# Kernel tuning notes

Measured on AMD Instinct MI355X. Metric: run time of the kernel, lower is better.

The kernel has to match this reference:

```python
import jax, jax.numpy as jnp
import numpy as np

N = 100000
E = 1600000
IN_DIM, HID, HEADS, OUT_DIM = 128, 64, 4, 40
NEG_SLOPE = 0.2
BN_EPS = 1e-5


def gat_conv(x, src, dst, W, att_src, att_dst, bias, heads, out_c, concat):
    # x: [N, F_in]; src/dst: [E'] (self-loops included)
    h = (x @ W).reshape(-1, heads, out_c)                      # [N, H, C]
    a_src = jnp.sum(h * att_src[None], axis=-1)                # [N, H]
    a_dst = jnp.sum(h * att_dst[None], axis=-1)                # [N, H]
    e = jax.nn.leaky_relu(a_src[src] + a_dst[dst], NEG_SLOPE)  # [E', H]
    # segment softmax over destination neighborhoods
    m = jax.ops.segment_max(e, dst, num_segments=N)            # [N, H]
    e = jnp.exp(e - m[dst])
    s = jax.ops.segment_sum(e, dst, num_segments=N)            # [N, H]
    alpha = e / (s[dst] + 1e-16)                               # [E', H]
    msg = h[src] * alpha[:, :, None]                           # [E', H, C]
    out = jax.ops.segment_sum(msg, dst, num_segments=N)        # [N, H, C]
    out = out.reshape(N, heads * out_c) if concat else out.mean(axis=1)
    return out + bias


def batch_norm(x, g, b, m, v):
    return (x - m) * (g / jnp.sqrt(v + BN_EPS)) + b


def setup_inputs() -> dict:
    key = jax.random.key(0)
    ks = jax.random.split(key, 16)
    rn = lambda k, shp, s=0.1: jax.random.normal(k, shp, jnp.float32) * s
    inp = {}
    inp['x'] = jax.random.normal(ks[0], (N, IN_DIM), jnp.float32)
    inp['edge_index'] = jax.random.randint(ks[1], (2, E), 0, N, jnp.int64)
    inp['W1'] = rn(ks[2], (IN_DIM, HEADS * HID))
    inp['att_src1'] = rn(ks[3], (HEADS, HID))
    inp['att_dst1'] = rn(ks[4], (HEADS, HID))
    inp['b1'] = rn(ks[5], (HEADS * HID,))
    inp['bn1_g'] = jax.random.uniform(ks[6], (HEADS * HID,), jnp.float32)
    inp['bn1_b'] = rn(ks[7], (HEADS * HID,))
    inp['bn1_m'] = jnp.zeros((HEADS * HID,), jnp.float32)
    inp['bn1_v'] = jnp.ones((HEADS * HID,), jnp.float32)
    inp['W2'] = rn(ks[8], (HEADS * HID, HID))
    inp['att_src2'] = rn(ks[9], (1, HID))
    inp['att_dst2'] = rn(ks[10], (1, HID))
    inp['b2'] = rn(ks[11], (HID,))
    inp['bn2_g'] = jax.random.uniform(ks[12], (HID,), jnp.float32)
    inp['bn2_b'] = rn(ks[13], (HID,))
    inp['bn2_m'] = jnp.zeros((HID,), jnp.float32)
    inp['bn2_v'] = jnp.ones((HID,), jnp.float32)
    inp['W3'] = rn(ks[14], (HID, OUT_DIM))
    k3 = jax.random.split(ks[15], 3)
    inp['att_src3'] = rn(k3[0], (1, OUT_DIM))
    inp['att_dst3'] = rn(k3[1], (1, OUT_DIM))
    inp['b3'] = rn(k3[2], (OUT_DIM,))
    return inp


def reference(x, edge_index, W1, att_src1, att_dst1, b1, bn1_g, bn1_b, bn1_m, bn1_v,
              W2, att_src2, att_dst2, b2, bn2_g, bn2_b, bn2_m, bn2_v,
              W3, att_src3, att_dst3, b3):
    # add self-loops (PyG GATConv default)
    loop = jnp.arange(N, dtype=edge_index.dtype)
    src = jnp.concatenate([edge_index[0], loop])
    dst = jnp.concatenate([edge_index[1], loop])
    # eval mode: dropout = identity, BN uses running stats
    h = gat_conv(x, src, dst, W1, att_src1, att_dst1, b1, HEADS, HID, True)
    h = jax.nn.elu(batch_norm(h, bn1_g, bn1_b, bn1_m, bn1_v))
    h = gat_conv(h, src, dst, W2, att_src2, att_dst2, b2, 1, HID, False)
    h = jax.nn.elu(batch_norm(h, bn2_g, bn2_b, bn2_m, bn2_v))
    out = gat_conv(h, src, dst, W3, att_src3, att_dst3, b3, 1, OUT_DIM, False)
    return jax.nn.log_softmax(out, axis=1)
```

## Files before the change

kernel.cpp:

```cpp
#include <hip/hip_runtime.h>
#include <hip/hip_fp16.h>
#include <cstdint>

#define IN_DIM   128
#define HIDC     64
#define HEADS    4
#define OUT_DIM  40
#define NEG_SLOPE 0.2f
#define BN_EPS   1e-5f

typedef unsigned short ushortt;
typedef float fx4 __attribute__((ext_vector_type(4)));

__device__ __forceinline__ float bfval(ushortt u) {
    return __uint_as_float(((unsigned)u) << 16);
}
__device__ __forceinline__ ushortt f2bf(float f) {
    unsigned u = __float_as_uint(f);
    u += 0x7fffu + ((u >> 16) & 1u);
    return (ushortt)(u >> 16);
}
__device__ __forceinline__ unsigned pack2bf(float a, float b) {
    return (unsigned)f2bf(a) | ((unsigned)f2bf(b) << 16);
}

__device__ __forceinline__ void acc8(float* acc, float a, uint4 h) {
    unsigned u;
    u = h.x;
    acc[0] = fmaf(a, __uint_as_float(u << 16), acc[0]);
    acc[1] = fmaf(a, __uint_as_float(u & 0xffff0000u), acc[1]);
    u = h.y;
    acc[2] = fmaf(a, __uint_as_float(u << 16), acc[2]);
    acc[3] = fmaf(a, __uint_as_float(u & 0xffff0000u), acc[3]);
    u = h.z;
    acc[4] = fmaf(a, __uint_as_float(u << 16), acc[4]);
    acc[5] = fmaf(a, __uint_as_float(u & 0xffff0000u), acc[5]);
    u = h.w;
    acc[6] = fmaf(a, __uint_as_float(u << 16), acc[6]);
    acc[7] = fmaf(a, __uint_as_float(u & 0xffff0000u), acc[7]);
}

__global__ void detect_kernel(const unsigned int* __restrict__ e, int* __restrict__ flag) {
    __shared__ int any;
    if (threadIdx.x == 0) any = 0;
    __syncthreads();
    for (int i = threadIdx.x; i < 1024; i += 256)
        if (e[2 * i + 1] != 0u) any = 1;
    __syncthreads();
    if (threadIdx.x == 0) flag[0] = any ? 0 : 1;
}

__device__ __forceinline__ int load_idx(const int* ei, int is64, long long pos) {
    return is64 ? ei[2 * pos] : ei[pos];
}

__global__ void hist_kernel(const int* __restrict__ ei, const int* __restrict__ flag,
                            int* __restrict__ deg, int E, int Etot) {
    int i = blockIdx.x * 256 + threadIdx.x;
    if (i >= Etot) return;
    int is64 = flag[0];
    int dst = (i < E) ? load_idx(ei, is64, (long long)E + i) : (i - E);
    atomicAdd(&deg[dst], 1);
}

__global__ void scan_kernel(int* __restrict__ data, int n) {
    __shared__ int wsum[16];
    __shared__ int chunk_total;
    int lane = threadIdx.x & 63;
    int w = threadIdx.x >> 6;
    int carry = 0;
    for (int base = 0; base < n; base += 1024) {
        int i = base + (int)threadIdx.x;
        int v = (i < n) ? data[i] : 0;
        int x = v;
        #pragma unroll
        for (int ofs = 1; ofs < 64; ofs <<= 1) {
            int y = __shfl_up(x, ofs);
            if (lane >= ofs) x += y;
        }
        if (lane == 63) wsum[w] = x;
        __syncthreads();
        if (w == 0) {
            int s = (lane < 16) ? wsum[lane] : 0;
            #pragma unroll
            for (int ofs = 1; ofs < 16; ofs <<= 1) {
                int y = __shfl_up(s, ofs);
                if (lane >= ofs) s += y;
            }
            if (lane < 16) wsum[lane] = s;
            if (lane == 15) chunk_total = s;
        }
        __syncthreads();
        int woff = (w > 0) ? wsum[w - 1] : 0;
        if (i < n) data[i] = (x + woff) - v + carry;
        int ct = chunk_total;
        __syncthreads();
        carry += ct;
    }
}

__global__ void scatter_kernel(const int* __restrict__ ei, const int* __restrict__ flag,
                               int* __restrict__ cursor, int* __restrict__ csr,
                               int* __restrict__ dstv, int E, int Etot) {
    int i = blockIdx.x * 256 + threadIdx.x;
    if (i >= Etot) return;
    int is64 = flag[0];
    int src, dst;
    if (i < E) {
        src = load_idx(ei, is64, i);
        dst = load_idx(ei, is64, (long long)E + i);
    } else {
        src = dst = i - E;
    }
    int pos = atomicAdd(&cursor[dst], 1);
    csr[pos] = src;
    dstv[pos] = dst;
}

__global__ void prep_bn_kernel(const float* b1, const float* g1, const float* bb1,
                               const float* m1, const float* v1,
                               const float* b2, const float* g2, const float* bb2,
                               const float* m2, const float* v2,
                               float* __restrict__ bnsc, float* __restrict__ bnsh) {
    int t = threadIdx.x;
    if (t < 256) {
        float s = g1[t] * rsqrtf(v1[t] + BN_EPS);
        bnsc[t] = s;
        bnsh[t] = (b1[t] - m1[t]) * s + bb1[t];
    } else if (t < 320) {
        int c = t - 256;
        float s = g2[c] * rsqrtf(v2[c] + BN_EPS);
        bnsc[t] = s;
        bnsh[t] = (b2[c] - m2[c]) * s + bb2[c];
    }
}

template <int K, int BN, int TN, int NC, int LDW, bool ABF16, bool L1MODE>
__launch_bounds__(256)
__global__ void gemm_fused_kernel(const void* __restrict__ Av, const float* __restrict__ W,
                                  ushortt* __restrict__ hB,
                                  const float* __restrict__ atts, const float* __restrict__ attd,
                                  float* __restrict__ a_s, float* __restrict__ a_d, int M) {
    __shared__ float Al[8][128];
    __shared__ float Wl[8][BN];
    int m0 = blockIdx.x * 128;
    int n0 = blockIdx.y * BN;
    int t = threadIdx.x;
    int tm = t >> 4, tn = t & 15;
    float acc[8][TN] = {};
    int r = t >> 1, kq = (t & 1) * 4;

    for (int k0 = 0; k0 < K; k0 += 8) {
        if constexpr (ABF16) {
            const ushortt* A = (const ushortt*)Av;
            uint2 av = make_uint2(0u, 0u);
            if (m0 + r < M) av = *(const uint2*)(A + (size_t)(m0 + r) * K + k0 + kq);
            Al[kq + 0][r] = bfval((ushortt)(av.x & 0xffffu));
            Al[kq + 1][r] = bfval((ushortt)(av.x >> 16));
            Al[kq + 2][r] = bfval((ushortt)(av.y & 0xffffu));
            Al[kq + 3][r] = bfval((ushortt)(av.y >> 16));
        } else {
            const float* A = (const float*)Av;
            float4 av = make_float4(0.f, 0.f, 0.f, 0.f);
            if (m0 + r < M) av = *(const float4*)&A[(size_t)(m0 + r) * K + k0 + kq];
            Al[kq + 0][r] = av.x; Al[kq + 1][r] = av.y;
            Al[kq + 2][r] = av.z; Al[kq + 3][r] = av.w;
        }
        if constexpr (BN == 128) {
            int kk = t >> 5, c4 = (t & 31) * 4;
            *(float4*)&Wl[kk][c4] = *(const float4*)&W[(size_t)(k0 + kk) * LDW + n0 + c4];
        } else {
            int kk = t >> 5, c2 = (t & 31) * 2;
            float2 wv = make_float2(0.f, 0.f);
            if (c2 + 2 <= NC) wv = *(const float2*)&W[(size_t)(k0 + kk) * LDW + n0 + c2];
            *(float2*)&Wl[kk][c2] = wv;
        }
        __syncthreads();
        #pragma unroll
        for (int k = 0; k < 8; ++k) {
            float4 a0 = *(const float4*)&Al[k][tm * 8];
            float4 a1 = *(const float4*)&Al[k][tm * 8 + 4];
            float aa[8] = {a0.x, a0.y, a0.z, a0.w, a1.x, a1.y, a1.z, a1.w};
            if constexpr (TN == 8) {
                float4 w0 = *(const float4*)&Wl[k][tn * 4];
                float4 w1 = *(const float4*)&Wl[k][64 + tn * 4];
                float ww[8] = {w0.x, w0.y, w0.z, w0.w, w1.x, w1.y, w1.z, w1.w};
                #pragma unroll
                for (int i = 0; i < 8; ++i)
                    #pragma unroll
                    for (int j = 0; j < 8; ++j)
                        acc[i][j] = fmaf(aa[i], ww[j], acc[i][j]);
            } else {
                float4 w0 = *(const float4*)&Wl[k][tn * 4];
                float ww[4] = {w0.x, w0.y, w0.z, w0.w};
                #pragma unroll
                for (int i = 0; i < 8; ++i)
                    #pragma unroll
                    for (int j = 0; j < 4; ++j)
                        acc[i][j] = fmaf(aa[i], ww[j], acc[i][j]);
            }
        }
        __syncthreads();
    }
    #pragma unroll
    for (int i = 0; i < 8; ++i) {
        int m = m0 + tm * 8 + i;
        bool valid = m < M;
        if constexpr (L1MODE) {
            int h0 = n0 >> 6;
            if (valid) {
                ushortt* row = hB + (size_t)m * 256 + n0;
                *(uint2*)(row + tn * 4) = make_uint2(pack2bf(acc[i][0], acc[i][1]),
                                                     pack2bf(acc[i][2], acc[i][3]));
                *(uint2*)(row + 64 + tn * 4) = make_uint2(pack2bf(acc[i][4], acc[i][5]),
                                                          pack2bf(acc[i][6], acc[i][7]));
            }
            int c0 = n0 + tn * 4, c1 = c0 + 64;
            float ps0 = acc[i][0] * atts[c0] + acc[i][1] * atts[c0 + 1]
                      + acc[i][2] * atts[c0 + 2] + acc[i][3] * atts[c0 + 3];
            float pd0 = acc[i][0] * attd[c0] + acc[i][1] * attd[c0 + 1]
                      + acc[i][2] * attd[c0 + 2] + acc[i][3] * attd[c0 + 3];
            float ps1 = acc[i][4] * atts[c1] + acc[i][5] * atts[c1 + 1]
                      + acc[i][6] * atts[c1 + 2] + acc[i][7] * atts[c1 + 3];
            float pd1 = acc[i][4] * attd[c1] + acc[i][5] * attd[c1 + 1]
                      + acc[i][6] * attd[c1 + 2] + acc[i][7] * attd[c1 + 3];
            #pragma unroll
            for (int o = 1; o < 16; o <<= 1) {
                ps0 += __shfl_xor(ps0, o); pd0 += __shfl_xor(pd0, o);
                ps1 += __shfl_xor(ps1, o); pd1 += __shfl_xor(pd1, o);
            }
            if (tn == 0 && valid) {
                a_s[(size_t)m * 4 + h0]     = ps0;
                a_s[(size_t)m * 4 + h0 + 1] = ps1;
                a_d[(size_t)m * 4 + h0]     = pd0;
                a_d[(size_t)m * 4 + h0 + 1] = pd1;
            }
        } else {
            if (valid) {
                ushortt* row = hB + (size_t)m * 64 + tn * 4;
                *(uint2*)row = make_uint2(pack2bf(acc[i][0], acc[i][1]),
                                          pack2bf(acc[i][2], acc[i][3]));
            }
            float ps = 0.f, pd = 0.f;
            #pragma unroll
            for (int j = 0; j < 4; ++j) {
                int c = tn * 4 + j;
                float as = (c < NC) ? atts[c] : 0.f;
                float ad = (c < NC) ? attd[c] : 0.f;
                ps = fmaf(acc[i][j], as, ps);
                pd = fmaf(acc[i][j], ad, pd);
            }
            #pragma unroll
            for (int o = 1; o < 16; o <<= 1) {
                ps += __shfl_xor(ps, o); pd += __shfl_xor(pd, o);
            }
            if (tn == 0 && valid) { a_s[m] = ps; a_d[m] = pd; }
        }
    }
}

__launch_bounds__(256)
__global__ void alpha4e_kernel(const int* __restrict__ csr, const int* __restrict__ dstv,
                               const float* __restrict__ a_s4, const float* __restrict__ a_d4,
                               __half* __restrict__ alH, int Etot) {
    int j = blockIdx.x * 256 + threadIdx.x;
    if (j >= Etot) return;
    int s = csr[j], d = dstv[j];
    fx4 as = *(const fx4*)&a_s4[(size_t)s * 4];
    fx4 ad = *(const fx4*)&a_d4[(size_t)d * 4];
    #pragma unroll
    for (int h = 0; h < 4; ++h) {
        float v = as[h] + ad[h];
        v = v > 0.f ? v : NEG_SLOPE * v;
        alH[(size_t)h * Etot + j] = __float2half(__expf(v));
    }
}

__launch_bounds__(256)
__global__ void pv1_kernel(const int* __restrict__ off, const int* __restrict__ csr,
                           const __half* __restrict__ alH, const ushortt* __restrict__ hB,
                           const float* __restrict__ bnsc, const float* __restrict__ bnsh,
                           ushortt* __restrict__ actb, int N, int Etot) {
    int node = blockIdx.x * 4 + (threadIdx.x >> 6);
    int lane = threadIdx.x & 63;
    if (node >= N) return;
    int half = lane >> 5, sub = lane & 31, head = sub >> 3;
    unsigned subb = (unsigned)(sub * 16);
    int beg = off[node], end = off[node + 1], deg = end - beg;
    const __half* alh = alH + (size_t)head * Etot;
    const char* hBb = (const char*)hB;
    float acc[8] = {};
    float ssum = 0.f;
    int nt = (deg + 1) >> 1;
    int j = beg + half;
    int t = 0;
    for (; t + 4 <= nt; t += 4, j += 8) {
        float av[4]; unsigned ro[4];
        #pragma unroll
        for (int q = 0; q < 4; ++q) {
            int jq = j + 2 * q;
            bool v = jq < end;
            int idx = v ? jq : beg;
            int s = csr[idx];
            av[q] = v ? __half2float(alh[idx]) : 0.f;
            ro[q] = (unsigned)s * 512u + subb;
        }
        uint4 h0 = *(const uint4*)(hBb + ro[0]);
        uint4 h1 = *(const uint4*)(hBb + ro[1]);
        uint4 h2 = *(const uint4*)(hBb + ro[2]);
        uint4 h3 = *(const uint4*)(hBb + ro[3]);
        acc8(acc, av[0], h0);
        acc8(acc, av[1], h1);
        acc8(acc, av[2], h2);
        acc8(acc, av[3], h3);
        ssum += (av[0] + av[1]) + (av[2] + av[3]);
    }
    for (; t < nt; ++t, j += 2) {
        bool v = j < end;
        int idx = v ? j : beg;
        int s = csr[idx];
        float a = v ? __half2float(alh[idx]) : 0.f;
        uint4 h = *(const uint4*)(hBb + (unsigned)s * 512u + subb);
        acc8(acc, a, h);
        ssum += a;
    }
    #pragma unroll
    for (int i = 0; i < 8; ++i) acc[i] += __shfl_xor(acc[i], 32);
    ssum += __shfl_xor(ssum, 32);
    if (half == 0) {
        float inv = 1.f / (ssum + 1e-16f);
        int g = sub * 8;
        float o[8];
        #pragma unroll
        for (int i = 0; i < 8; ++i) {
            float v = acc[i] * inv * bnsc[g + i] + bnsh[g + i];
            o[i] = v > 0.f ? v : expm1f(v);
        }
        uint4 pk = make_uint4(pack2bf(o[0], o[1]), pack2bf(o[2], o[3]),
                              pack2bf(o[4], o[5]), pack2bf(o[6], o[7]));
        *(uint4*)&actb[(size_t)node * 256 + g] = pk;
    }
}

__launch_bounds__(256)
__global__ void pv2_kernel(const int* __restrict__ off, const int* __restrict__ csr,
                           const float* __restrict__ a_s, const float* __restrict__ a_d,
                           const ushortt* __restrict__ hB,
                           const float* __restrict__ bnsc, const float* __restrict__ bnsh,
                           ushortt* __restrict__ act2b, int N) {
    int node = blockIdx.x * 4 + (threadIdx.x >> 6);
    int lane = threadIdx.x & 63;
    if (node >= N) return;
    int grp = lane >> 3, sub = lane & 7;
    unsigned subb = (unsigned)(sub * 16);
    int beg = off[node], end = off[node + 1], deg = end - beg;
    float ad = a_d[node];
    const char* hBb = (const char*)hB;
    float acc[8] = {};
    float ssum = 0.f;
    int nt = (deg + 7) >> 3;
    int j = beg + grp;
    int t = 0;
    for (; t + 2 <= nt; t += 2, j += 16) {
        int jA = j, jB = j + 8;
        bool vA = jA < end, vB = jB < end;
        int iA = vA ? jA : beg, iB = vB ? jB : beg;
        int sA = csr[iA], sB = csr[iB];
        float wA = a_s[sA] + ad; wA = wA > 0.f ? wA : NEG_SLOPE * wA;
        float wB = a_s[sB] + ad; wB = wB > 0.f ? wB : NEG_SLOPE * wB;
        float aA = vA ? __expf(wA) : 0.f;
        float aB = vB ? __expf(wB) : 0.f;
        uint4 hA = *(const uint4*)(hBb + (unsigned)sA * 128u + subb);
        uint4 hBv = *(const uint4*)(hBb + (unsigned)sB * 128u + subb);
        acc8(acc, aA, hA);
        acc8(acc, aB, hBv);
        ssum += aA + aB;
    }
    for (; t < nt; ++t, j += 8) {
        bool v = j < end;
        int idx = v ? j : beg;
        int s = csr[idx];
        float w = a_s[s] + ad; w = w > 0.f ? w : NEG_SLOPE * w;
        float a = v ? __expf(w) : 0.f;
        uint4 h = *(const uint4*)(hBb + (unsigned)s * 128u + subb);
        acc8(acc, a, h);
        ssum += a;
    }
    #pragma unroll
    for (int o = 8; o <= 32; o <<= 1) {
        #pragma unroll
        for (int i = 0; i < 8; ++i) acc[i] += __shfl_xor(acc[i], o);
        ssum += __shfl_xor(ssum, o);
    }
    if (lane < 8) {
        float inv = 1.f / (ssum + 1e-16f);
        int g = lane * 8;
        float o[8];
        #pragma unroll
        for (int i = 0; i < 8; ++i) {
            float v = acc[i] * inv * bnsc[256 + g + i] + bnsh[256 + g + i];
            o[i] = v > 0.f ? v : expm1f(v);
        }
        uint4 pk = make_uint4(pack2bf(o[0], o[1]), pack2bf(o[2], o[3]),
                              pack2bf(o[4], o[5]), pack2bf(o[6], o[7]));
        *(uint4*)&act2b[(size_t)node * 64 + g] = pk;
    }
}

__launch_bounds__(256)
__global__ void pv3_kernel(const int* __restrict__ off, const int* __restrict__ csr,
                           const float* __restrict__ a_s, const float* __restrict__ a_d,
                           const ushortt* __restrict__ hB, const float* __restrict__ bias,
                           float* __restrict__ out, int N) {
    int node = blockIdx.x * 4 + (threadIdx.x >> 6);
    int lane = threadIdx.x & 63;
    if (node >= N) return;
    int grp = lane >> 3, sub = lane & 7;
    unsigned subb = (unsigned)(sub * 16);
    int beg = off[node], end = off[node + 1];
    float ad = a_d[node];
    const char* hBb = (const char*)hB;
    float acc[8] = {};
    float ssum = 0.f;
    for (int j0 = beg; j0 < end; j0 += 8) {
        int j = j0 + grp;
        bool v = j < end;
        int idx = v ? j : beg;
        int s = csr[idx];
        float w = a_s[s] + ad; w = w > 0.f ? w : NEG_SLOPE * w;
        float a = v ? __expf(w) : 0.f;
        uint4 h = *(const uint4*)(hBb + (unsigned)s * 128u + subb);
        acc8(acc, a, h);
        ssum += a;
    }
    #pragma unroll
    for (int o = 8; o <= 32; o <<= 1) {
        #pragma unroll
        for (int i = 0; i < 8; ++i) acc[i] += __shfl_xor(acc[i], o);
        ssum += __shfl_xor(ssum, o);
    }
    float inv = 1.f / (ssum + 1e-16f);
    int g = lane * 8;
    bool act8 = lane < 5;
    float val[8];
    float mx = -INFINITY;
    #pragma unroll
    for (int i = 0; i < 8; ++i) {
        val[i] = act8 ? (acc[i] * inv + bias[act8 ? (g + i) : 0]) : -INFINITY;
        mx = fmaxf(mx, val[i]);
    }
    #pragma unroll
    for (int o = 1; o < 8; o <<= 1) mx = fmaxf(mx, __shfl_xor(mx, o));
    float se = 0.f;
    if (act8) {
        #pragma unroll
        for (int i = 0; i < 8; ++i) se += __expf(val[i] - mx);
    }
    #pragma unroll
    for (int o = 1; o < 8; o <<= 1) se += __shfl_xor(se, o);
    if (act8) {
        float lse = mx + logf(se);
        float* dst = &out[(size_t)node * 40 + g];
        fx4 v0 = {val[0] - lse, val[1] - lse, val[2] - lse, val[3] - lse};
        fx4 v1 = {val[4] - lse, val[5] - lse, val[6] - lse, val[7] - lse};
        *(fx4*)dst = v0;
        *(fx4*)(dst + 4) = v1;
    }
}

extern "C" void kernel_launch(void* const* d_in, const int* in_sizes, int n_in,
                              void* d_out, int out_size, void* d_ws, size_t ws_size,
                              hipStream_t stream) {
    const float* x      = (const float*)d_in[0];
    const int*   ei     = (const int*)d_in[1];
    const float* W1     = (const float*)d_in[2];
    const float* att_s1 = (const float*)d_in[3];
    const float* att_d1 = (const float*)d_in[4];
    const float* b1     = (const float*)d_in[5];
    const float* bn1g   = (const float*)d_in[6];
    const float* bn1b   = (const float*)d_in[7];
    const float* bn1m   = (const float*)d_in[8];
    const float* bn1v   = (const float*)d_in[9];
    const float* W2     = (const float*)d_in[10];
    const float* att_s2 = (const float*)d_in[11];
    const float* att_d2 = (const float*)d_in[12];
    const float* b2     = (const float*)d_in[13];
    const float* bn2g   = (const float*)d_in[14];
    const float* bn2b   = (const float*)d_in[15];
    const float* bn2m   = (const float*)d_in[16];
    const float* bn2v   = (const float*)d_in[17];
    const float* W3     = (const float*)d_in[18];
    const float* att_s3 = (const float*)d_in[19];
    const float* att_d3 = (const float*)d_in[20];
    const float* b3     = (const float*)d_in[21];

    const int N    = in_sizes[0] / IN_DIM;
    const int E    = in_sizes[1] / 2;
    const int Etot = E + N;

    int*   wsi = (int*)d_ws;
    float* wsf = (float*)d_ws;
    size_t p = 0;
    int*   off    = wsi + p; p += (size_t)N + 16;  p = (p + 3) & ~(size_t)3;
    int*   cursor = wsi + p; p += (size_t)N;       p = (p + 3) & ~(size_t)3;
    int*   flag   = wsi + p; p += 16;
    int*   csr    = wsi + p; p += (size_t)Etot;    p = (p + 3) & ~(size_t)3;
    int*   dstv   = wsi + p; p += (size_t)Etot;    p = (p + 3) & ~(size_t)3;
    float* a_s4   = wsf + p; p += (size_t)N * 4;
    float* a_d4   = wsf + p; p += (size_t)N * 4;
    float* bnsc   = wsf + p; p += 384;
    float* bnsh   = wsf + p; p += 384;
    size_t H = p;            p += (size_t)N * 128;
    size_t A1 = p;           p += (size_t)N * 128;
    size_t A2 = p;           p += (size_t)N * 32;
    __half* alH = (__half*)(wsf + p); p += (size_t)Etot * 2 + 16;
    if (ws_size < p * 4) return;

    ushortt* hB1   = (ushortt*)(wsf + H);
    ushortt* hB23  = (ushortt*)(wsf + H);
    ushortt* actb  = (ushortt*)(wsf + A1);
    ushortt* act2b = (ushortt*)(wsf + A2);

    float* outp = (float*)d_out;

    hipMemsetAsync(off, 0, ((size_t)N + 1) * sizeof(int), stream);
    detect_kernel<<<1, 256, 0, stream>>>((const unsigned int*)ei, flag);
    {
        int blocks = (Etot + 255) / 256;
        hist_kernel<<<blocks, 256, 0, stream>>>(ei, flag, off, E, Etot);
        scan_kernel<<<1, 1024, 0, stream>>>(off, N + 1);
        hipMemcpyAsync(cursor, off, (size_t)N * sizeof(int), hipMemcpyDeviceToDevice, stream);
        scatter_kernel<<<blocks, 256, 0, stream>>>(ei, flag, cursor, csr, dstv, E, Etot);
    }
    prep_bn_kernel<<<1, 384, 0, stream>>>(b1, bn1g, bn1b, bn1m, bn1v,
                                          b2, bn2g, bn2b, bn2m, bn2v, bnsc, bnsh);

    const int gm = (N + 127) / 128;
    const int nb4 = (N + 3) / 4;
    const int eb = (Etot + 255) / 256;

    gemm_fused_kernel<128, 128, 8, 256, 256, false, true>
        <<<dim3(gm, 2), 256, 0, stream>>>(x, W1, hB1, att_s1, att_d1, a_s4, a_d4, N);
    alpha4e_kernel<<<eb, 256, 0, stream>>>(csr, dstv, a_s4, a_d4, alH, Etot);
    pv1_kernel<<<nb4, 256, 0, stream>>>(off, csr, alH, hB1, bnsc, bnsh, actb, N, Etot);

    gemm_fused_kernel<256, 64, 4, 64, 64, true, false>
        <<<dim3(gm, 1), 256, 0, stream>>>(actb, W2, hB23, att_s2, att_d2, a_s4, a_d4, N);
    pv2_kernel<<<nb4, 256, 0, stream>>>(off, csr, a_s4, a_d4, hB23, bnsc, bnsh, act2b, N);

    gemm_fused_kernel<64, 64, 4, 40, 40, true, false>
        <<<dim3(gm, 1), 256, 0, stream>>>(act2b, W3, hB23, att_s3, att_d3, a_s4, a_d4, N);
    pv3_kernel<<<nb4, 256, 0, stream>>>(off, csr, a_s4, a_d4, hB23, b3, outp, N);
}
```

Measured before the change: 776.0 us.

## Use bf16 MFMA for GAT linear layers and precompute per-edge attention weights

Replaces the FP32 register-tiled GEMMs with a bf16 MFMA 16x16x32 kernel. To feed it, x is cast to bf16 and the weights are transposed and cast. Layers 2 and 3 now compute exp(leaky_relu) per edge in a separate pass stored as fp16, instead of recomputing it inside the aggregation kernels. This cuts FP32 FMA cost in the GEMMs and removes the gather of a_s plus the exp in the aggregation loops. In exchange it adds extra launches, extra edge-array traffic, and bf16 rounding of the input x.

Result: faster. 704.4 us (-9.2%).

```diff
diff --git a/kernel.cpp b/kernel.cpp
--- a/kernel.cpp
+++ b/kernel.cpp
@@ -11,6 +11,7 @@
 
 typedef unsigned short ushortt;
 typedef float fx4 __attribute__((ext_vector_type(4)));
+typedef short bf16x8 __attribute__((ext_vector_type(8)));
 
 __device__ __forceinline__ float bfval(ushortt u) {
     return __uint_as_float(((unsigned)u) << 16);
@@ -135,126 +136,96 @@
     }
 }
 
-template <int K, int BN, int TN, int NC, int LDW, bool ABF16, bool L1MODE>
+__global__ void castx_kernel(const float* __restrict__ x, ushortt* __restrict__ xb, int n8) {
+    int i = blockIdx.x * 256 + threadIdx.x;
+    if (i >= n8) return;
+    const float4* src = (const float4*)(x + (size_t)i * 8);
+    float4 v0 = src[0], v1 = src[1];
+    uint4 pk = make_uint4(pack2bf(v0.x, v0.y), pack2bf(v0.z, v0.w),
+                          pack2bf(v1.x, v1.y), pack2bf(v1.z, v1.w));
+    *(uint4*)(xb + (size_t)i * 8) = pk;
+}
+
+__global__ void prep_wt_kernel(const float* __restrict__ W, ushortt* __restrict__ WT,
+                               int K, int Norig, int Npad) {
+    int i = blockIdx.x * 256 + threadIdx.x;
+    if (i >= K * Npad) return;
+    int n = i / K, k = i % K;
+    WT[i] = (n < Norig) ? f2bf(W[(size_t)k * Norig + n]) : (ushortt)0;
+}
+
+template <int K, int NCATT, bool L1MODE>
 __launch_bounds__(256)
-__global__ void gemm_fused_kernel(const void* __restrict__ Av, const float* __restrict__ W,
-                                  ushortt* __restrict__ hB,
-                                  const float* __restrict__ atts, const float* __restrict__ attd,
-                                  float* __restrict__ a_s, float* __restrict__ a_d, int M) {
-    __shared__ float Al[8][128];
-    __shared__ float Wl[8][BN];
-    int m0 = blockIdx.x * 128;
-    int n0 = blockIdx.y * BN;
+__global__ void gemm_mfma_kernel(const ushortt* __restrict__ A, const ushortt* __restrict__ BT,
+                                 ushortt* __restrict__ hB,
+                                 const float* __restrict__ atts, const float* __restrict__ attd,
+                                 float* __restrict__ a_s, float* __restrict__ a_d, int M) {
+    __shared__ ushortt Abuf[64][40];
+    __shared__ ushortt Bbuf[64][40];
+    int m0 = blockIdx.x * 64;
+    int head = L1MODE ? blockIdx.y : 0;
+    int n0g = head * 64;
     int t = threadIdx.x;
-    int tm = t >> 4, tn = t & 15;
-    float acc[8][TN] = {};
-    int r = t >> 1, kq = (t & 1) * 4;
-
-    for (int k0 = 0; k0 < K; k0 += 8) {
-        if constexpr (ABF16) {
-            const ushortt* A = (const ushortt*)Av;
-            uint2 av = make_uint2(0u, 0u);
-            if (m0 + r < M) av = *(const uint2*)(A + (size_t)(m0 + r) * K + k0 + kq);
-            Al[kq + 0][r] = bfval((ushortt)(av.x & 0xffffu));
-            Al[kq + 1][r] = bfval((ushortt)(av.x >> 16));
-            Al[kq + 2][r] = bfval((ushortt)(av.y & 0xffffu));
-            Al[kq + 3][r] = bfval((ushortt)(av.y >> 16));
-        } else {
-            const float* A = (const float*)Av;
-            float4 av = make_float4(0.f, 0.f, 0.f, 0.f);
-            if (m0 + r < M) av = *(const float4*)&A[(size_t)(m0 + r) * K + k0 + kq];
-            Al[kq + 0][r] = av.x; Al[kq + 1][r] = av.y;
-            Al[kq + 2][r] = av.z; Al[kq + 3][r] = av.w;
-        }
-        if constexpr (BN == 128) {
-            int kk = t >> 5, c4 = (t & 31) * 4;
-            *(float4*)&Wl[kk][c4] = *(const float4*)&W[(size_t)(k0 + kk) * LDW + n0 + c4];
-        } else {
-            int kk = t >> 5, c2 = (t & 31) * 2;
-            float2 wv = make_float2(0.f, 0.f);
-            if (c2 + 2 <= NC) wv = *(const float2*)&W[(size_t)(k0 + kk) * LDW + n0 + c2];
-            *(float2*)&Wl[kk][c2] = wv;
-        }
+    int w = t >> 6, l = t & 63;
+    int colg = l & 15, kg = l >> 4;
+    int srow = t >> 2, sseg = t & 3;
+
+    fx4 acc[4] = {};
+
+    for (int k0 = 0; k0 < K; k0 += 32) {
+        uint4 av = make_uint4(0u, 0u, 0u, 0u);
+        if (m0 + srow < M)
+            av = *(const uint4*)(A + (size_t)(m0 + srow) * K + k0 + sseg * 8);
+        *(uint4*)&Abuf[srow][sseg * 8] = av;
+        uint4 bv = *(const uint4*)(BT + (size_t)(n0g + srow) * K + k0 + sseg * 8);
+        *(uint4*)&Bbuf[srow][sseg * 8] = bv;
         __syncthreads();
-        #pragma unroll
-        for (int k = 0; k < 8; ++k) {
-            float4 a0 = *(const float4*)&Al[k][tm * 8];
-            float4 a1 = *(const float4*)&Al[k][tm * 8 + 4];
-            float aa[8] = {a0.x, a0.y, a0.z, a0.w, a1.x, a1.y, a1.z, a1.w};
-            if constexpr (TN == 8) {
-                float4 w0 = *(const float4*)&Wl[k][tn * 4];
-                float4 w1 = *(const float4*)&Wl[k][64 + tn * 4];
-                float ww[8] = {w0.x, w0.y, w0.z, w0.w, w1.x, w1.y, w1.z, w1.w};
-                #pragma unroll
-                for (int i = 0; i < 8; ++i)
-                    #pragma unroll
-                    for (int j = 0; j < 8; ++j)
-                        acc[i][j] = fmaf(aa[i], ww[j], acc[i][j]);
-            } else {
-                float4 w0 = *(const float4*)&Wl[k][tn * 4];
-                float ww[4] = {w0.x, w0.y, w0.z, w0.w};
-                #pragma unroll
-                for (int i = 0; i < 8; ++i)
-                    #pragma unroll
-                    for (int j = 0; j < 4; ++j)
-                        acc[i][j] = fmaf(aa[i], ww[j], acc[i][j]);
+        bf16x8 a = *(const bf16x8*)&Abuf[w * 16 + colg][kg * 8];
+        #pragma unroll
+        for (int bt = 0; bt < 4; ++bt) {
+            bf16x8 b = *(const bf16x8*)&Bbuf[bt * 16 + colg][kg * 8];
+            acc[bt] = __builtin_amdgcn_mfma_f32_16x16x32_bf16(a, b, acc[bt], 0, 0, 0);
+        }
+        __syncthreads();
+    }
+
+    const int nstride = L1MODE ? 256 : 64;
+    float ps[4] = {}, pd[4] = {};
+    #pragma unroll
+    for (int bt = 0; bt < 4; ++bt) {
+        int cl = bt * 16 + colg;
+        float as_v = (cl < NCATT) ? atts[n0g + cl] : 0.f;
+        float ad_v = (cl < NCATT) ? attd[n0g + cl] : 0.f;
+        #pragma unroll
+        for (int i = 0; i < 4; ++i) {
+            int m = m0 + w * 16 + kg * 4 + i;
+            if (m < M)
+                hB[(size_t)m * nstride + n0g + cl] = f2bf(acc[bt][i]);
+            ps[i] = fmaf(acc[bt][i], as_v, ps[i]);
+            pd[i] = fmaf(acc[bt][i], ad_v, pd[i]);
+        }
+    }
+    #pragma unroll
+    for (int o = 1; o < 16; o <<= 1) {
+        #pragma unroll
+        for (int i = 0; i < 4; ++i) {
+            ps[i] += __shfl_xor(ps[i], o);
+            pd[i] += __shfl_xor(pd[i], o);
+        }
+    }
+    if (colg == 0) {
+        #pragma unroll
+        for (int i = 0; i < 4; ++i) {
+            int m = m0 + w * 16 + kg * 4 + i;
+            if (m < M) {
+                if constexpr (L1MODE) {
+                    a_s[(size_t)m * 4 + head] = ps[i];
+                    a_d[(size_t)m * 4 + head] = pd[i];
+                } else {
+                    a_s[m] = ps[i];
+                    a_d[m] = pd[i];
+                }
             }
-        }
-        __syncthreads();
-    }
-    #pragma unroll
-    for (int i = 0; i < 8; ++i) {
-        int m = m0 + tm * 8 + i;
-        bool valid = m < M;
-        if constexpr (L1MODE) {
-            int h0 = n0 >> 6;
-            if (valid) {
-                ushortt* row = hB + (size_t)m * 256 + n0;
-                *(uint2*)(row + tn * 4) = make_uint2(pack2bf(acc[i][0], acc[i][1]),
-                                                     pack2bf(acc[i][2], acc[i][3]));
-                *(uint2*)(row + 64 + tn * 4) = make_uint2(pack2bf(acc[i][4], acc[i][5]),
-                                                          pack2bf(acc[i][6], acc[i][7]));
-            }
-            int c0 = n0 + tn * 4, c1 = c0 + 64;
-            float ps0 = acc[i][0] * atts[c0] + acc[i][1] * atts[c0 + 1]
-                      + acc[i][2] * atts[c0 + 2] + acc[i][3] * atts[c0 + 3];
-            float pd0 = acc[i][0] * attd[c0] + acc[i][1] * attd[c0 + 1]
-                      + acc[i][2] * attd[c0 + 2] + acc[i][3] * attd[c0 + 3];
-            float ps1 = acc[i][4] * atts[c1] + acc[i][5] * atts[c1 + 1]
-                      + acc[i][6] * atts[c1 + 2] + acc[i][7] * atts[c1 + 3];
-            float pd1 = acc[i][4] * attd[c1] + acc[i][5] * attd[c1 + 1]
-                      + acc[i][6] * attd[c1 + 2] + acc[i][7] * attd[c1 + 3];
-            #pragma unroll
-            for (int o = 1; o < 16; o <<= 1) {
-                ps0 += __shfl_xor(ps0, o); pd0 += __shfl_xor(pd0, o);
-                ps1 += __shfl_xor(ps1, o); pd1 += __shfl_xor(pd1, o);
-            }
-            if (tn == 0 && valid) {
-                a_s[(size_t)m * 4 + h0]     = ps0;
-                a_s[(size_t)m * 4 + h0 + 1] = ps1;
-                a_d[(size_t)m * 4 + h0]     = pd0;
-                a_d[(size_t)m * 4 + h0 + 1] = pd1;
-            }
-        } else {
-            if (valid) {
-                ushortt* row = hB + (size_t)m * 64 + tn * 4;
-                *(uint2*)row = make_uint2(pack2bf(acc[i][0], acc[i][1]),
-                                          pack2bf(acc[i][2], acc[i][3]));
-            }
-            float ps = 0.f, pd = 0.f;
-            #pragma unroll
-            for (int j = 0; j < 4; ++j) {
-                int c = tn * 4 + j;
-                float as = (c < NC) ? atts[c] : 0.f;
-                float ad = (c < NC) ? attd[c] : 0.f;
-                ps = fmaf(acc[i][j], as, ps);
-                pd = fmaf(acc[i][j], ad, pd);
-            }
-            #pragma unroll
-            for (int o = 1; o < 16; o <<= 1) {
-                ps += __shfl_xor(ps, o); pd += __shfl_xor(pd, o);
-            }
-            if (tn == 0 && valid) { a_s[m] = ps; a_d[m] = pd; }
         }
     }
 }
@@ -274,6 +245,17 @@
         v = v > 0.f ? v : NEG_SLOPE * v;
         alH[(size_t)h * Etot + j] = __float2half(__expf(v));
     }
+}
+
+__launch_bounds__(256)
+__global__ void alpha1e_kernel(const int* __restrict__ csr, const int* __restrict__ dstv,
+                               const float* __restrict__ a_s, const float* __restrict__ a_d,
+                               __half* __restrict__ alE, int Etot) {
+    int j = blockIdx.x * 256 + threadIdx.x;
+    if (j >= Etot) return;
+    float v = a_s[csr[j]] + a_d[dstv[j]];
+    v = v > 0.f ? v : NEG_SLOPE * v;
+    alE[j] = __float2half(__expf(v));
 }
 
 __launch_bounds__(256)
@@ -344,8 +326,7 @@
 
 __launch_bounds__(256)
 __global__ void pv2_kernel(const int* __restrict__ off, const int* __restrict__ csr,
-                           const float* __restrict__ a_s, const float* __restrict__ a_d,
-                           const ushortt* __restrict__ hB,
+                           const __half* __restrict__ alE, const ushortt* __restrict__ hB,
                            const float* __restrict__ bnsc, const float* __restrict__ bnsh,
                            ushortt* __restrict__ act2b, int N) {
     int node = blockIdx.x * 4 + (threadIdx.x >> 6);
@@ -354,7 +335,6 @@
     int grp = lane >> 3, sub = lane & 7;
     unsigned subb = (unsigned)(sub * 16);
     int beg = off[node], end = off[node + 1], deg = end - beg;
-    float ad = a_d[node];
     const char* hBb = (const char*)hB;
     float acc[8] = {};
     float ssum = 0.f;
@@ -366,10 +346,8 @@
         bool vA = jA < end, vB = jB < end;
         int iA = vA ? jA : beg, iB = vB ? jB : beg;
         int sA = csr[iA], sB = csr[iB];
-        float wA = a_s[sA] + ad; wA = wA > 0.f ? wA : NEG_SLOPE * wA;
-        float wB = a_s[sB] + ad; wB = wB > 0.f ? wB : NEG_SLOPE * wB;
-        float aA = vA ? __expf(wA) : 0.f;
-        float aB = vB ? __expf(wB) : 0.f;
+        float aA = vA ? __half2float(alE[iA]) : 0.f;
+        float aB = vB ? __half2float(alE[iB]) : 0.f;
         uint4 hA = *(const uint4*)(hBb + (unsigned)sA * 128u + subb);
         uint4 hBv = *(const uint4*)(hBb + (unsigned)sB * 128u + subb);
         acc8(acc, aA, hA);
@@ -380,8 +358,7 @@
         bool v = j < end;
         int idx = v ? j : beg;
         int s = csr[idx];
-        float w = a_s[s] + ad; w = w > 0.f ? w : NEG_SLOPE * w;
-        float a = v ? __expf(w) : 0.f;
+        float a = v ? __half2float(alE[idx]) : 0.f;
         uint4 h = *(const uint4*)(hBb + (unsigned)s * 128u + subb);
         acc8(acc, a, h);
         ssum += a;
@@ -409,16 +386,14 @@
 
 __launch_bounds__(256)
 __global__ void pv3_kernel(const int* __restrict__ off, const int* __restrict__ csr,
-                           const float* __restrict__ a_s, const float* __restrict__ a_d,
-                           const ushortt* __restrict__ hB, const float* __restrict__ bias,
-                           float* __restrict__ out, int N) {
+                           const __half* __restrict__ alE, const ushortt* __restrict__ hB,
+                           const float* __restrict__ bias, float* __restrict__ out, int N) {
     int node = blockIdx.x * 4 + (threadIdx.x >> 6);
     int lane = threadIdx.x & 63;
     if (node >= N) return;
     int grp = lane >> 3, sub = lane & 7;
     unsigned subb = (unsigned)(sub * 16);
     int beg = off[node], end = off[node + 1];
-    float ad = a_d[node];
     const char* hBb = (const char*)hB;
     float acc[8] = {};
     float ssum = 0.f;
@@ -427,8 +402,7 @@
         bool v = j < end;
         int idx = v ? j : beg;
         int s = csr[idx];
-        float w = a_s[s] + ad; w = w > 0.f ? w : NEG_SLOPE * w;
-        float a = v ? __expf(w) : 0.f;
+        float a = v ? __half2float(alE[idx]) : 0.f;
         uint4 h = *(const uint4*)(hBb + (unsigned)s * 128u + subb);
         acc8(acc, a, h);
         ssum += a;
@@ -510,6 +484,10 @@
     float* a_d4   = wsf + p; p += (size_t)N * 4;
     float* bnsc   = wsf + p; p += 384;
     float* bnsh   = wsf + p; p += 384;
+    ushortt* xb   = (ushortt*)(wsf + p); p += (size_t)N * 64;
+    ushortt* W1T  = (ushortt*)(wsf + p); p += (256 * 128) / 2 + 16;
+    ushortt* W2T  = (ushortt*)(wsf + p); p += (64 * 256) / 2 + 16;
+    ushortt* W3T  = (ushortt*)(wsf + p); p += (64 * 64) / 2 + 16;
     size_t H = p;            p += (size_t)N * 128;
     size_t A1 = p;           p += (size_t)N * 128;
     size_t A2 = p;           p += (size_t)N * 32;
@@ -520,6 +498,7 @@
     ushortt* hB23  = (ushortt*)(wsf + H);
     ushortt* actb  = (ushortt*)(wsf + A1);
     ushortt* act2b = (ushortt*)(wsf + A2);
+    __half*  alE   = alH;
 
     float* outp = (float*)d_out;
 
@@ -534,21 +513,27 @@
     }
     prep_bn_kernel<<<1, 384, 0, stream>>>(b1, bn1g, bn1b, bn1m, bn1v,
                                           b2, bn2g, bn2b, bn2m, bn2v, bnsc, bnsh);
-
-    const int gm = (N + 127) / 128;
+    prep_wt_kernel<<<(256 * 128 + 255) / 256, 256, 0, stream>>>(W1, W1T, 128, 256, 256);
+    prep_wt_kernel<<<(64 * 256 + 255) / 256, 256, 0, stream>>>(W2, W2T, 256, 64, 64);
+    prep_wt_kernel<<<(64 * 64 + 255) / 256, 256, 0, stream>>>(W3, W3T, 64, 40, 64);
+    castx_kernel<<<((N * 16) + 255) / 256, 256, 0, stream>>>(x, xb, N * 16);
+
+    const int gm64 = (N + 63) / 64;
     const int nb4 = (N + 3) / 4;
     const int eb = (Etot + 255) / 256;
 
-    gemm_fused_kernel<128, 128, 8, 256, 256, false, true>
-        <<<dim3(gm, 2), 256, 0, stream>>>(x, W1, hB1, att_s1, att_d1, a_s4, a_d4, N);
+    gemm_mfma_kernel<128, 64, true>
+        <<<dim3(gm64, 4), 256, 0, stream>>>(xb, W1T, hB1, att_s1, att_d1, a_s4, a_d4, N);
     alpha4e_kernel<<<eb, 256, 0, stream>>>(csr, dstv, a_s4, a_d4, alH, Etot);
     pv1_kernel<<<nb4, 256, 0, stream>>>(off, csr, alH, hB1, bnsc, bnsh, actb, N, Etot);
 
-    gemm_fused_kernel<256, 64, 4, 64, 64, true, false>
-        <<<dim3(gm, 1), 256, 0, stream>>>(actb, W2, hB23, att_s2, att_d2, a_s4, a_d4, N);
-    pv2_kernel<<<nb4, 256, 0, stream>>>(off, csr, a_s4, a_d4, hB23, bnsc, bnsh, act2b, N);
-
-    gemm_fused_kernel<64, 64, 4, 40, 40, true, false>
-        <<<dim3(gm, 1), 256, 0, stream>>>(act2b, W3, hB23, att_s3, att_d3, a_s4, a_d4, N);
-    pv3_kernel<<<nb4, 256, 0, stream>>>(off, csr, a_s4, a_d4, hB23, b3, outp, N);
-}
+    gemm_mfma_kernel<256, 64, false>
+        <<<dim3(gm64, 1), 256, 0, stream>>>(actb, W2T, hB23, att_s2, att_d2, a_s4, a_d4, N);
+    alpha1e_kernel<<<eb, 256, 0, stream>>>(csr, dstv, a_s4, a_d4, alE, Etot);
+    pv2_kernel<<<nb4, 256, 0, stream>>>(off, csr, alE, hB23, bnsc, bnsh, act2b, N);
+
+    gemm_mfma_kernel<64, 40, false>
+        <<<dim3(gm64, 1), 256, 0, stream>>>(act2b, W3T, hB23, att_s3, att_d3, a_s4, a_d4, N);
+    alpha1e_kernel<<<eb, 256, 0, stream>>>(csr, dstv, a_s4, a_d4, alE, Etot);
+    pv3_kernel<<<nb4, 256, 0, stream>>>(off, csr, alE, hB23, b3, outp, N);
+}
```
